# Performance work log

Measured on AMD Instinct MI355X. Metric: run time of the kernel, lower is better.

Reference implementation:

```python
import jax, jax.numpy as jnp
import numpy as np

N, T, F_IN = 20000, 6, 64   # nodes, seq_len, in_channels
E = 320000                  # edges (avg degree 16)
H, C = 4, 64                # gat1 heads, hidden_channels


def setup_inputs() -> dict:
    key = jax.random.key(0)
    ks = jax.random.split(key, 16)
    p = lambda i, shape, s=0.1: jax.random.normal(ks[i], shape, jnp.float32) * s
    return dict(
        x=p(0, (N, T, F_IN), 1.0),
        edge_index=jax.random.randint(ks[1], (2, E), 0, N),
        # GATv2 layer 1: in=F_IN, out=C per head, H heads, concat
        Wl1=p(2, (F_IN, H * C)), Wr1=p(3, (F_IN, H * C)), att1=p(4, (H, C)), b1=jnp.zeros((H * C,), jnp.float32),
        # GATv2 layer 2: in=H*C, out=C, 1 head, no concat
        Wl2=p(5, (H * C, C)), Wr2=p(6, (H * C, C)), att2=p(7, (1, C)), b2=jnp.zeros((C,), jnp.float32),
        # LSTM (input C, hidden C), pytorch gate order i,f,g,o
        Wih=p(8, (4 * C, C)), Whh=p(9, (4 * C, C)), bih=jnp.zeros((4 * C,), jnp.float32), bhh=jnp.zeros((4 * C,), jnp.float32),
        # MLP head
        Wfc1=p(10, (C, C // 2)), bfc1=jnp.zeros((C // 2,), jnp.float32),
        Wout=p(11, (C // 2, 1)), bout=jnp.zeros((1,), jnp.float32),
    )


def gatv2(xt, src, dst, Wl, Wr, att, bias, n):
    """GATv2Conv (eval mode, no edge_attr): gather -> attn -> segment-softmax -> scatter."""
    heads = att.shape[0]
    d = Wl.shape[1] // heads
    xl = (xt @ Wl).reshape(n, heads, d)   # source transform
    xr = (xt @ Wr).reshape(n, heads, d)   # target transform
    e = jax.nn.leaky_relu(xl[src] + xr[dst], 0.2)           # [E, heads, d]
    logit = jnp.einsum('ehc,hc->eh', e, att)                # [E, heads]
    m = jax.ops.segment_max(logit, dst, num_segments=n)      # per-target max
    ex = jnp.exp(logit - m[dst])
    denom = jax.ops.segment_sum(ex, dst, num_segments=n)
    alpha = ex / denom[dst]                                  # segment softmax
    out = jax.ops.segment_sum(alpha[:, :, None] * xl[src], dst, num_segments=n)
    return out.reshape(n, heads * d) + bias


def reference(x, edge_index, Wl1, Wr1, att1, b1, Wl2, Wr2, att2, b2,
              Wih, Whh, bih, bhh, Wfc1, bfc1, Wout, bout):
    src, dst = edge_index[0], edge_index[1]
    n = x.shape[0]

    def gat_step(carry, xt):                    # per-timestep spatial encoder
        h1 = jax.nn.elu(gatv2(xt, src, dst, Wl1, Wr1, att1, b1, n))
        h2 = jax.nn.elu(gatv2(h1, src, dst, Wl2, Wr2, att2, b2, n))
        return carry, h2

    _, seq = jax.lax.scan(gat_step, 0.0, jnp.swapaxes(x, 0, 1))  # [T, N, C]

    hid = Whh.shape[1]

    def lstm_step(carry, xt):
        h, c = carry
        g = xt @ Wih.T + bih + h @ Whh.T + bhh
        i, f, gg, o = jnp.split(g, 4, axis=-1)
        c = jax.nn.sigmoid(f) * c + jax.nn.sigmoid(i) * jnp.tanh(gg)
        h = jax.nn.sigmoid(o) * jnp.tanh(c)
        return (h, c), None

    h0 = jnp.zeros((n, hid), x.dtype)
    (h_last, _), _ = jax.lax.scan(lstm_step, (h0, h0), seq)

    z = jax.nn.relu(h_last @ Wfc1 + bfc1)
    return z @ Wout + bout
```

## Files before the change

### kernel.cpp

```cpp
#include <hip/hip_runtime.h>
#include <hip/hip_fp16.h>
#include <math.h>

#define N_NODES 20000
#define T_STEPS 6
#define F_INCH  64
#define HC      256
#define CH      64

typedef _Float16 h8    __attribute__((ext_vector_type(8)));
typedef _Float16 hv2   __attribute__((ext_vector_type(2)));
typedef float    f32x4 __attribute__((ext_vector_type(4)));

__device__ __forceinline__ float fast_tanh(float x){
  float e = __expf(2.f*x);
  return 1.f - 2.f/(e + 1.f);
}

__device__ __forceinline__ float fdot2v(hv2 a, hv2 b, float c){
#if __has_builtin(__builtin_amdgcn_fdot2)
  return __builtin_amdgcn_fdot2(a, b, c, false);
#else
  return fmaf((float)a[0], (float)b[0], fmaf((float)a[1], (float)b[1], c));
#endif
}

__device__ __forceinline__ hv2 leaky2(hv2 t){
  hv2 s = t * (_Float16)0.2f;
#if __has_builtin(__builtin_elementwise_max)
  return __builtin_elementwise_max(t, s);
#else
  hv2 r;
  r[0] = (t[0] > s[0]) ? t[0] : s[0];
  r[1] = (t[1] > s[1]) ? t[1] : s[1];
  return r;
#endif
}

__global__ void k_count(const int* __restrict__ dst, int E, int* __restrict__ deg){
  int e = blockIdx.x*256 + threadIdx.x;
  if (e < E) atomicAdd(&deg[dst[e]], 1);
}

__global__ void k_scan(const int* __restrict__ deg, int* __restrict__ row_start, int N){
  __shared__ int wsum[16];
  const int PT = 20;
  int tid = threadIdx.x, wid = tid >> 6, lane = tid & 63;
  int base = tid*PT;
  int loc[PT];
  int s = 0;
  #pragma unroll
  for (int j = 0; j < PT; j++){
    int i = base + j;
    int v = (i < N) ? deg[i] : 0;
    loc[j] = s;
    s += v;
  }
  int ss = s;
  #pragma unroll
  for (int off = 1; off < 64; off <<= 1){
    int t = __shfl_up(ss, off, 64);
    if (lane >= off) ss += t;
  }
  if (lane == 63) wsum[wid] = ss;
  __syncthreads();
  if (tid < 16){
    int w = wsum[tid];
    #pragma unroll
    for (int off = 1; off < 16; off <<= 1){
      int t = __shfl_up(w, off, 64);
      if (tid >= off) w += t;
    }
    wsum[tid] = w;
  }
  __syncthreads();
  int pre = ((wid ? wsum[wid-1] : 0)) + (ss - s);
  #pragma unroll
  for (int j = 0; j < PT; j++){
    int i = base + j;
    if (i < N) row_start[i] = pre + loc[j];
  }
  if (tid == 0) row_start[N] = wsum[15];
}

__global__ void k_scatter(const int* __restrict__ src, const int* __restrict__ dst, int E,
                          const int* __restrict__ row_start, int* __restrict__ cursor,
                          int* __restrict__ csr){
  int e = blockIdx.x*256 + threadIdx.x;
  if (e < E){
    int d = dst[e];
    int pos = atomicAdd(&cursor[d], 1);
    csr[row_start[d] + pos] = src[e];
  }
}

__global__ void k_sort(const int* __restrict__ row_start, int* __restrict__ csr, int N){
  int wid = threadIdx.x >> 6, lane = threadIdx.x & 63;
  int d = blockIdx.x*4 + wid;
  if (d >= N) return;
  int s = row_start[d], e = row_start[d+1], len = e - s;
  if (len <= 1) return;
  if (len <= 64){
    int v = (lane < len) ? csr[s + lane] : 0x7fffffff;
    int rank = 0;
    for (int j = 0; j < len; j++){
      int vj = __shfl(v, j, 64);
      rank += (int)((vj < v) | ((vj == v) & (j < lane)));
    }
    if (lane < len) csr[s + rank] = v;
  } else if (lane == 0){
    for (int i = s+1; i < e; i++){
      int key = csr[i]; int j = i-1;
      while (j >= s && csr[j] > key){ csr[j+1] = csr[j]; j--; }
      csr[j+1] = key;
    }
  }
}

__device__ __forceinline__ void packB_dev(const float* __restrict__ B, _Float16* __restrict__ Bf,
                                          int K, int N, int idx){
  if (idx >= K*N) return;
  int j    = idx & 7;
  int lane = (idx >> 3) & 63;
  int ntk  = idx >> 9;
  int NT = N >> 4;
  int ks = ntk / NT, nt = ntk - ks*NT;
  int k = ks*32 + ((lane >> 4) << 3) + j;
  int n = nt*16 + (lane & 15);
  Bf[idx] = (_Float16)B[k*N + n];
}

__device__ __forceinline__ void packBT_dev(const float* __restrict__ W, _Float16* __restrict__ Bf,
                                           int K, int N, int idx){
  if (idx >= K*N) return;
  int j    = idx & 7;
  int lane = (idx >> 3) & 63;
  int ntk  = idx >> 9;
  int NT = N >> 4;
  int ks = ntk / NT, nt = ntk - ks*NT;
  int k = ks*32 + ((lane >> 4) << 3) + j;
  int n = nt*16 + (lane & 15);
  Bf[idx] = (_Float16)W[n*K + k];
}

__global__ void k_packall(const float* __restrict__ bih, const float* __restrict__ bhh,
                          float* __restrict__ biasc,
                          const float* __restrict__ Wl1, _Float16* __restrict__ Bl1f,
                          const float* __restrict__ Wr1, _Float16* __restrict__ Br1f,
                          const float* __restrict__ Wl2, _Float16* __restrict__ Bl2f,
                          const float* __restrict__ Wr2, _Float16* __restrict__ Br2f,
                          const float* __restrict__ Wih, _Float16* __restrict__ Wihf,
                          const float* __restrict__ Whh, _Float16* __restrict__ Whhf){
  int grp = blockIdx.x >> 6;
  int idx = (blockIdx.x & 63)*256 + threadIdx.x;
  if (grp == 0){
    if (idx < 256) biasc[idx] = bih[idx] + bhh[idx];
  } else if (grp == 1){
    packB_dev(Wl1, Bl1f, 64, 256, idx);
  } else if (grp == 2){
    packB_dev(Wr1, Br1f, 64, 256, idx);
  } else if (grp == 3){
    packB_dev(Wl2, Bl2f, 256, 64, idx);
  } else if (grp == 4){
    packB_dev(Wr2, Br2f, 256, 64, idx);
  } else if (grp == 5){
    packBT_dev(Wih, Wihf, 64, 256, idx);
  } else {
    packBT_dev(Whh, Whhf, 64, 256, idx);
  }
}

__global__ __launch_bounds__(256) void k_gemm1_all(
    const float* __restrict__ x, const _Float16* __restrict__ B1f,
    const _Float16* __restrict__ B2f,
    __half* __restrict__ xl_all, __half* __restrict__ xr_all, int M){
  __shared__ _Float16 aT[32*72];
  int t = blockIdx.y;
  const float* A = x + t*F_INCH;
  _Float16* C1 = (_Float16*)(void*)xl_all + (size_t)t*N_NODES*HC;
  _Float16* C2 = (_Float16*)(void*)xr_all + (size_t)t*N_NODES*HC;
  int tid = threadIdx.x;
  int r0 = blockIdx.x*32;
  for (int i = tid; i < 32*64; i += 256){
    int r = i >> 6, k = i & 63;
    int row = r0 + r;
    aT[r*72 + k] = (row < M) ? (_Float16)A[(size_t)row*(T_STEPS*F_INCH) + k] : (_Float16)0.f;
  }
  __syncthreads();
  int wave = tid >> 6, lane = tid & 63;
  int m = wave & 1;
  const h8* Bfrag = (const h8*)((wave >> 1) ? B2f : B1f);
  _Float16* C = (wave >> 1) ? C2 : C1;
  int arow = m*16 + (lane & 15);
  int kb = (lane >> 4) * 8;
  h8 a0 = *(const h8*)&aT[arow*72 + kb];
  h8 a1 = *(const h8*)&aT[arow*72 + 32 + kb];
  f32x4 z = {0.f, 0.f, 0.f, 0.f};
  f32x4 acc[16];
  #pragma unroll
  for (int nt = 0; nt < 16; nt++) acc[nt] = z;
  #pragma unroll
  for (int nt = 0; nt < 16; nt++){
    h8 b0 = Bfrag[nt*64 + lane];
    h8 b1 = Bfrag[(16 + nt)*64 + lane];
    acc[nt] = __builtin_amdgcn_mfma_f32_16x16x32_f16(a0, b0, acc[nt], 0, 0, 0);
    acc[nt] = __builtin_amdgcn_mfma_f32_16x16x32_f16(a1, b1, acc[nt], 0, 0, 0);
  }
  int ccol = lane & 15, crow = (lane >> 4) * 4;
  #pragma unroll
  for (int nt = 0; nt < 16; nt++){
    #pragma unroll
    for (int r = 0; r < 4; r++){
      int row = r0 + m*16 + crow + r;
      if (row < M) C[(size_t)row*256 + nt*16 + ccol] = (_Float16)acc[nt][r];
    }
  }
}

__global__ __launch_bounds__(256) void k_gemm2_all(
    const __half* __restrict__ Aall, const _Float16* __restrict__ B1f,
    const _Float16* __restrict__ B2f,
    __half* __restrict__ C1h_all, __half* __restrict__ C2h_all, int M){
  __shared__ _Float16 aT[32*264];
  int t = blockIdx.y;
  const _Float16* A = (const _Float16*)(const void*)Aall + (size_t)t*N_NODES*HC;
  _Float16* C1 = (_Float16*)(void*)C1h_all + (size_t)t*N_NODES*CH;
  _Float16* C2 = (_Float16*)(void*)C2h_all + (size_t)t*N_NODES*CH;
  int tid = threadIdx.x;
  int r0 = blockIdx.x*32;
  h8 zh = {(_Float16)0.f,(_Float16)0.f,(_Float16)0.f,(_Float16)0.f,
           (_Float16)0.f,(_Float16)0.f,(_Float16)0.f,(_Float16)0.f};
  for (int i = tid; i < 32*32; i += 256){
    int r = i >> 5, c = i & 31;
    int row = r0 + r;
    h8 v = zh;
    if (row < M) v = *(const h8*)&A[(size_t)row*256 + c*8];
    *(h8*)&aT[r*264 + c*8] = v;
  }
  __syncthreads();
  int wave = tid >> 6, lane = tid & 63;
  int m = wave & 1;
  const h8* Bfrag = (const h8*)((wave >> 1) ? B2f : B1f);
  _Float16* C = (wave >> 1) ? C2 : C1;
  int arow = m*16 + (lane & 15);
  int kb = (lane >> 4) * 8;
  f32x4 z = {0.f, 0.f, 0.f, 0.f};
  f32x4 acc[4];
  #pragma unroll
  for (int nt = 0; nt < 4; nt++) acc[nt] = z;
  #pragma unroll
  for (int ks = 0; ks < 8; ks++){
    h8 a = *(const h8*)&aT[arow*264 + ks*32 + kb];
    #pragma unroll
    for (int nt = 0; nt < 4; nt++){
      h8 b = Bfrag[(ks*4 + nt)*64 + lane];
      acc[nt] = __builtin_amdgcn_mfma_f32_16x16x32_f16(a, b, acc[nt], 0, 0, 0);
    }
  }
  int ccol = lane & 15, crow = (lane >> 4) * 4;
  #pragma unroll
  for (int nt = 0; nt < 4; nt++){
    #pragma unroll
    for (int r = 0; r < 4; r++){
      int row = r0 + m*16 + crow + r;
      if (row < M) C[(size_t)row*64 + nt*16 + ccol] = (_Float16)acc[nt][r];
    }
  }
}

__global__ void k_gat1_all(const __half* __restrict__ xl_all, const __half* __restrict__ xr_all,
                           const int* __restrict__ row_start, const int* __restrict__ csr,
                           const float* __restrict__ att, const float* __restrict__ bias,
                           __half* __restrict__ out_all, int N){
  int wid = threadIdx.x >> 6, lane = threadIdx.x & 63;
  int dst = blockIdx.x*4 + wid;
  if (dst >= N) return;
  int t = blockIdx.y;
  const char* xlb = (const char*)(xl_all + (size_t)t*N_NODES*HC);
  const uint2* xrh = (const uint2*)(xr_all + (size_t)t*N_NODES*HC);
  uint2* outh = (uint2*)(out_all + (size_t)t*N_NODES*HC);
  uint2 xr_raw = xrh[(unsigned)(dst*64 + lane)];
  hv2 xr01 = *reinterpret_cast<hv2*>(&xr_raw.x);
  hv2 xr23 = *reinterpret_cast<hv2*>(&xr_raw.y);
  float4 at4 = ((const float4*)att)[lane];
  hv2 at01; at01[0] = (_Float16)at4.x; at01[1] = (_Float16)at4.y;
  hv2 at23; at23[0] = (_Float16)at4.z; at23[1] = (_Float16)at4.w;
  unsigned loff = lane*8u;
  int s0 = __builtin_amdgcn_readfirstlane(row_start[dst]);
  int s1 = __builtin_amdgcn_readfirstlane(row_start[dst+1]);
  float den = 0.f, ax = 0.f, ay = 0.f, az = 0.f, aw = 0.f;

  auto STEP = [&](uint2 raw){
    hv2 h01 = *reinterpret_cast<hv2*>(&raw.x);
    hv2 h23 = *reinterpret_cast<hv2*>(&raw.y);
    hv2 l01 = leaky2(h01 + xr01);
    hv2 l23 = leaky2(h23 + xr23);
    float p = fdot2v(l01, at01, fdot2v(l23, at23, 0.f));
    p += __shfl_xor(p, 1, 64);
    p += __shfl_xor(p, 2, 64);
    p += __shfl_xor(p, 4, 64);
    p += __shfl_xor(p, 8, 64);
    float w = __expf(p);
    den += w;
    ax = fmaf(w, (float)h01[0], ax);
    ay = fmaf(w, (float)h01[1], ay);
    az = fmaf(w, (float)h23[0], az);
    aw = fmaf(w, (float)h23[1], aw);
  };

  for (int base = s0; base < s1; base += 64){
    int rem = s1 - base;
    int cnt = rem < 64 ? rem : 64;
    int idxv = (base + lane < s1) ? csr[base + lane] : 0;
    auto LD = [&](int i)->uint2 {
      int s = __builtin_amdgcn_readlane(idxv, i & 63);
      return *(const uint2*)(xlb + (((size_t)(unsigned)s) << 9) + loff);
    };
    uint2 p0=LD(0), p1=LD(1), p2=LD(2), p3=LD(3);
    uint2 p4=LD(4), p5=LD(5), p6=LD(6), p7=LD(7);
    for (int i = 0; i < cnt; i += 4){
      uint2 n0=LD(i+8), n1=LD(i+9), n2=LD(i+10), n3=LD(i+11);
      if (i + 4 <= cnt){
        STEP(p0); STEP(p1); STEP(p2); STEP(p3);
      } else {
        STEP(p0);
        if (i+1 < cnt) STEP(p1);
        if (i+2 < cnt) STEP(p2);
        if (i+3 < cnt) STEP(p3);
      }
      p0=p4; p1=p5; p2=p6; p3=p7;
      p4=n0; p5=n1; p6=n2; p7=n3;
    }
  }
  float invd = (s1 > s0) ? 1.f/den : 0.f;
  float4 b4 = ((const float4*)bias)[lane];
  float rx = fmaf(ax, invd, b4.x);
  float ry = fmaf(ay, invd, b4.y);
  float rz = fmaf(az, invd, b4.z);
  float rw = fmaf(aw, invd, b4.w);
  rx = rx > 0.f ? rx : (__expf(rx) - 1.f);
  ry = ry > 0.f ? ry : (__expf(ry) - 1.f);
  rz = rz > 0.f ? rz : (__expf(rz) - 1.f);
  rw = rw > 0.f ? rw : (__expf(rw) - 1.f);
  __half2 o01 = __floats2half2_rn(rx, ry);
  __half2 o23 = __floats2half2_rn(rz, rw);
  uint2 o;
  o.x = *reinterpret_cast<unsigned int*>(&o01);
  o.y = *reinterpret_cast<unsigned int*>(&o23);
  outh[(unsigned)(dst*64 + lane)] = o;
}

__global__ void k_gat2_all(const __half* __restrict__ xl_all, const __half* __restrict__ xr_all,
                           const int* __restrict__ row_start, const int* __restrict__ csr,
                           const float* __restrict__ att, const float* __restrict__ bias,
                           __half* __restrict__ out_all, int N){
  int wid = threadIdx.x >> 6, lane = threadIdx.x & 63;
  int dst = blockIdx.x*4 + wid;
  if (dst >= N) return;
  int t = blockIdx.y;
  int g = lane >> 4, q = lane & 15;
  const char* xlb = (const char*)(xl_all + (size_t)t*N_NODES*CH);
  const uint2* xrh = (const uint2*)(xr_all + (size_t)t*N_NODES*CH);
  uint2* outh = (uint2*)(out_all + (size_t)t*N_NODES*CH);
  uint2 xr_raw = xrh[(unsigned)(dst*16 + q)];
  hv2 xr01 = *reinterpret_cast<hv2*>(&xr_raw.x);
  hv2 xr23 = *reinterpret_cast<hv2*>(&xr_raw.y);
  float4 at4 = ((const float4*)att)[q];
  hv2 at01; at01[0] = (_Float16)at4.x; at01[1] = (_Float16)at4.y;
  hv2 at23; at23[0] = (_Float16)at4.z; at23[1] = (_Float16)at4.w;
  unsigned qoff = q*8u;
  int s0 = __builtin_amdgcn_readfirstlane(row_start[dst]);
  int s1 = __builtin_amdgcn_readfirstlane(row_start[dst+1]);
  float den = 0.f, ax = 0.f, ay = 0.f, az = 0.f, aw = 0.f;

  for (int base = s0; base < s1; base += 64){
    int rem = s1 - base;
    int cnt = rem < 64 ? rem : 64;
    int idxv = (base + lane < s1) ? csr[base + lane] : 0;
    int K = (cnt + 3) >> 2;
    int e0 = g, e1 = g + 4;
    int sA = __shfl(idxv, e0 < cnt ? e0 : 0, 64);
    int sB = __shfl(idxv, e1 < cnt ? e1 : 0, 64);
    uint2 vA = *(const uint2*)(xlb + (((size_t)(unsigned)sA) << 7) + qoff);
    uint2 vB = *(const uint2*)(xlb + (((size_t)(unsigned)sB) << 7) + qoff);
    for (int k = 0; k < K; k++){
      int en = 4*k + 8 + g;
      int sN = __shfl(idxv, en < cnt ? en : 0, 64);
      uint2 vN = *(const uint2*)(xlb + (((size_t)(unsigned)sN) << 7) + qoff);
      int e = 4*k + g;
      if (e < cnt){
        hv2 h01 = *reinterpret_cast<hv2*>(&vA.x);
        hv2 h23 = *reinterpret_cast<hv2*>(&vA.y);
        hv2 l01 = leaky2(h01 + xr01);
        hv2 l23 = leaky2(h23 + xr23);
        float p = fdot2v(l01, at01, fdot2v(l23, at23, 0.f));
        p += __shfl_xor(p, 1, 64);
        p += __shfl_xor(p, 2, 64);
        p += __shfl_xor(p, 4, 64);
        p += __shfl_xor(p, 8, 64);
        float w = __expf(p);
        den += w;
        ax = fmaf(w, (float)h01[0], ax);
        ay = fmaf(w, (float)h01[1], ay);
        az = fmaf(w, (float)h23[0], az);
        aw = fmaf(w, (float)h23[1], aw);
      }
      vA = vB; vB = vN;
    }
  }
  den += __shfl_xor(den, 16, 64); den += __shfl_xor(den, 32, 64);
  ax  += __shfl_xor(ax, 16, 64);  ax  += __shfl_xor(ax, 32, 64);
  ay  += __shfl_xor(ay, 16, 64);  ay  += __shfl_xor(ay, 32, 64);
  az  += __shfl_xor(az, 16, 64);  az  += __shfl_xor(az, 32, 64);
  aw  += __shfl_xor(aw, 16, 64);  aw  += __shfl_xor(aw, 32, 64);
  float invd = (s1 > s0) ? 1.f/den : 0.f;
  float4 b4 = ((const float4*)bias)[q];
  float rx = fmaf(ax, invd, b4.x);
  float ry = fmaf(ay, invd, b4.y);
  float rz = fmaf(az, invd, b4.z);
  float rw = fmaf(aw, invd, b4.w);
  rx = rx > 0.f ? rx : (__expf(rx) - 1.f);
  ry = ry > 0.f ? ry : (__expf(ry) - 1.f);
  rz = rz > 0.f ? rz : (__expf(rz) - 1.f);
  rw = rw > 0.f ? rw : (__expf(rw) - 1.f);
  if (g == 0){
    __half2 o01 = __floats2half2_rn(rx, ry);
    __half2 o23 = __floats2half2_rn(rz, rw);
    uint2 o;
    o.x = *reinterpret_cast<unsigned int*>(&o01);
    o.y = *reinterpret_cast<unsigned int*>(&o23);
    outh[(unsigned)(dst*16 + q)] = o;
  }
}

__global__ __launch_bounds__(256) void k_gemmx_all(
    const __half* __restrict__ Aall, const _Float16* __restrict__ Bf,
    const float* __restrict__ biasc, __half* __restrict__ Call){
  __shared__ _Float16 aT[32*72];
  int tid = threadIdx.x;
  int r0 = blockIdx.x*32;
  {
    int r = tid >> 3, c8 = tid & 7;
    *(h8*)&aT[r*72 + c8*8] =
        *(const h8*)&((const _Float16*)(const void*)Aall)[((size_t)(r0+r))*64 + c8*8];
  }
  __syncthreads();
  int wave = tid >> 6, lane = tid & 63;
  int m = wave & 1, nh = wave >> 1;
  int arow = m*16 + (lane & 15);
  int kb = (lane >> 4) * 8;
  h8 a0 = *(const h8*)&aT[arow*72 + kb];
  h8 a1 = *(const h8*)&aT[arow*72 + 32 + kb];
  const h8* B = (const h8*)Bf;
  f32x4 z = {0.f, 0.f, 0.f, 0.f};
  f32x4 acc[8];
  #pragma unroll
  for (int nt = 0; nt < 8; nt++) acc[nt] = z;
  #pragma unroll
  for (int nt = 0; nt < 8; nt++){
    int ntg = nh*8 + nt;
    acc[nt] = __builtin_amdgcn_mfma_f32_16x16x32_f16(a0, B[ntg*64 + lane],        acc[nt], 0,0,0);
    acc[nt] = __builtin_amdgcn_mfma_f32_16x16x32_f16(a1, B[(16 + ntg)*64 + lane], acc[nt], 0,0,0);
  }
  int ccol = lane & 15, crow = (lane >> 4) * 4;
  _Float16* C = (_Float16*)(void*)Call;
  #pragma unroll
  for (int nt = 0; nt < 8; nt++){
    int ntg = nh*8 + nt;
    int col = ntg*16 + ccol;
    float b = biasc[col];
    #pragma unroll
    for (int r = 0; r < 4; r++){
      C[(size_t)(r0 + m*16 + crow + r)*256 + col] = (_Float16)(acc[nt][r] + b);
    }
  }
}

__global__ __launch_bounds__(64) void k_lstm_rec(
    const __half* __restrict__ gatesx,
    const _Float16* __restrict__ Whhf,
    const float* __restrict__ Wfc1, const float* __restrict__ bfc1,
    const float* __restrict__ Wout, const float* __restrict__ bout,
    float* __restrict__ out, int N){
  __shared__ _Float16 gxT[16*264];
  __shared__ _Float16 hT[16*68];
  int lane = threadIdx.x;
  int r0 = blockIdx.x*16;
  for (int i = lane; i < 16*68; i += 64) hT[i] = (_Float16)0.f;
  int ccol = lane & 15, crow = (lane >> 4) * 4;
  int arow_off = (lane & 15)*68 + ((lane >> 4) << 3);
  const h8* Bfrag = (const h8*)Whhf;
  const _Float16* gxb = (const _Float16*)(const void*)gatesx;
  float c[16];
  #pragma unroll
  for (int i = 0; i < 16; i++) c[i] = 0.f;

  for (int t = 0; t < T_STEPS; t++){
    const _Float16* gx = gxb + ((size_t)t*N_NODES + r0)*256;
    #pragma unroll
    for (int it = 0; it < 8; it++){
      int idx = it*64 + lane;
      int r = idx >> 5, c8 = idx & 31;
      *(h8*)&gxT[r*264 + c8*8] = *(const h8*)&gx[(size_t)r*256 + c8*8];
    }
    h8 a0 = *(const h8*)&hT[arow_off];
    h8 a1 = *(const h8*)&hT[arow_off + 32];
    f32x4 z = {0.f, 0.f, 0.f, 0.f};
    f32x4 acc[16];
    #pragma unroll
    for (int nt = 0; nt < 16; nt++) acc[nt] = z;
    #pragma unroll
    for (int nt = 0; nt < 16; nt++){
      acc[nt] = __builtin_amdgcn_mfma_f32_16x16x32_f16(a0, Bfrag[nt*64 + lane],        acc[nt], 0,0,0);
      acc[nt] = __builtin_amdgcn_mfma_f32_16x16x32_f16(a1, Bfrag[(16 + nt)*64 + lane], acc[nt], 0,0,0);
    }
    #pragma unroll
    for (int us = 0; us < 4; us++){
      int ucol = us*16 + ccol;
      #pragma unroll
      for (int r = 0; r < 4; r++){
        int row = crow + r;
        float gi = acc[us     ][r] + (float)gxT[row*264 +       ucol];
        float gf = acc[4  + us][r] + (float)gxT[row*264 +  64 + ucol];
        float gg = acc[8  + us][r] + (float)gxT[row*264 + 128 + ucol];
        float go = acc[12 + us][r] + (float)gxT[row*264 + 192 + ucol];
        float I = 1.f/(1.f + __expf(-gi));
        float F = 1.f/(1.f + __expf(-gf));
        float O = 1.f/(1.f + __expf(-go));
        float G = fast_tanh(gg);
        float cc = fmaf(F, c[us*4 + r], I*G);
        c[us*4 + r] = cc;
        hT[row*68 + ucol] = (_Float16)(O * fast_tanh(cc));
      }
    }
  }
  int rowm = lane >> 2;
  int cb = (lane & 3) * 8;
  float a8[8];
  #pragma unroll
  for (int j = 0; j < 8; j++) a8[j] = bfc1[cb + j];
  for (int k = 0; k < 64; k++){
    float hv = (float)hT[rowm*68 + k];
    #pragma unroll
    for (int j = 0; j < 8; j++) a8[j] = fmaf(hv, Wfc1[k*32 + cb + j], a8[j]);
  }
  float v = 0.f;
  #pragma unroll
  for (int j = 0; j < 8; j++) v += fmaxf(a8[j], 0.f) * Wout[cb + j];
  v += __shfl_xor(v, 1, 64);
  v += __shfl_xor(v, 2, 64);
  if ((lane & 3) == 0) out[r0 + rowm] = v + bout[0];
}

extern "C" void kernel_launch(void* const* d_in, const int* in_sizes, int n_in,
                              void* d_out, int out_size, void* d_ws, size_t ws_size,
                              hipStream_t stream){
  const float* x    = (const float*)d_in[0];
  const int*   edge = (const int*)  d_in[1];
  const float* Wl1  = (const float*)d_in[2];
  const float* Wr1  = (const float*)d_in[3];
  const float* att1 = (const float*)d_in[4];
  const float* b1   = (const float*)d_in[5];
  const float* Wl2  = (const float*)d_in[6];
  const float* Wr2  = (const float*)d_in[7];
  const float* att2 = (const float*)d_in[8];
  const float* b2   = (const float*)d_in[9];
  const float* Wih  = (const float*)d_in[10];
  const float* Whh  = (const float*)d_in[11];
  const float* bih  = (const float*)d_in[12];
  const float* bhh  = (const float*)d_in[13];
  const float* Wfc1 = (const float*)d_in[14];
  const float* bfc1 = (const float*)d_in[15];
  const float* Wout = (const float*)d_in[16];
  const float* bout = (const float*)d_in[17];
  float* out = (float*)d_out;

  const int N = N_NODES;
  const int E = in_sizes[1] / 2;

  char* p = (char*)d_ws;
  auto alloc = [&](size_t bytes)->char*{ char* q = p; p += (bytes + 255) & ~(size_t)255; return q; };
  int* csr       = (int*)alloc((size_t)E*sizeof(int));
  int* row_start = (int*)alloc((size_t)(N+1)*sizeof(int));
  int* deg       = (int*)alloc((size_t)N*sizeof(int));
  int* cursor    = (int*)alloc((size_t)N*sizeof(int));
  const size_t NB = (size_t)T_STEPS*N_NODES*HC;
  char* bufA = alloc(NB*2);
  char* bufB = alloc(NB*2);
  char* bufC = alloc(NB*2);
  float* biasc  = (float*)alloc(256*4);
  _Float16* Bl1f = (_Float16*)alloc(64*256*2);
  _Float16* Br1f = (_Float16*)alloc(64*256*2);
  _Float16* Bl2f = (_Float16*)alloc(256*64*2);
  _Float16* Br2f = (_Float16*)alloc(256*64*2);
  _Float16* Wihf = (_Float16*)alloc(64*256*2);
  _Float16* Whhf = (_Float16*)alloc(64*256*2);

  __half* xl1h_all = (__half*)bufA;
  __half* xr1h_all = (__half*)bufB;
  __half* h1_all   = (__half*)bufC;
  __half* xl2h_all = (__half*)bufA;
  __half* xr2h_all = (__half*)(bufA + (size_t)T_STEPS*N_NODES*CH*2);
  __half* h2f_all  = (__half*)bufB;
  __half* gatesx   = (__half*)bufC;

  const int* srcIdx = edge;
  const int* dstIdx = edge + E;

  hipMemsetAsync(deg, 0, (size_t)((char*)cursor - (char*)deg) + (size_t)N*4, stream);

  k_count  <<<(E+255)/256, 256, 0, stream>>>(dstIdx, E, deg);
  k_scan   <<<1, 1024, 0, stream>>>(deg, row_start, N);
  k_scatter<<<(E+255)/256, 256, 0, stream>>>(srcIdx, dstIdx, E, row_start, cursor, csr);
  k_sort   <<<(N+3)/4, 256, 0, stream>>>(row_start, csr, N);
  k_packall<<<448, 256, 0, stream>>>(bih, bhh, biasc,
                                     Wl1, Bl1f, Wr1, Br1f, Wl2, Bl2f, Wr2, Br2f,
                                     Wih, Wihf, Whh, Whhf);

  dim3 gGemm((N+31)/32, T_STEPS);
  dim3 gGat ((N+3)/4,  T_STEPS);
  k_gemm1_all<<<gGemm, 256, 0, stream>>>(x, Bl1f, Br1f, xl1h_all, xr1h_all, N);
  k_gat1_all <<<gGat,  256, 0, stream>>>(xl1h_all, xr1h_all, row_start, csr, att1, b1, h1_all, N);
  k_gemm2_all<<<gGemm, 256, 0, stream>>>(h1_all, Bl2f, Br2f, xl2h_all, xr2h_all, N);
  k_gat2_all <<<gGat,  256, 0, stream>>>(xl2h_all, xr2h_all, row_start, csr, att2, b2, h2f_all, N);

  k_gemmx_all<<<(T_STEPS*N)/32, 256, 0, stream>>>(h2f_all, Wihf, biasc, gatesx);
  k_lstm_rec <<<N/16, 64, 0, stream>>>(gatesx, Whhf, Wfc1, bfc1, Wout, bout, out, N);
}
```

Before: 403.3 us.

## Fuse LSTM input projection into recurrent kernel with concatenated Wih|Whh weights

Removes the separate gates-x GEMM kernel and its fp16 [T,N,256] intermediate. Each LSTM step now runs one K=128 MFMA over the concatenated [x_t, h] tile against a packed Wih|Whh matrix, with the bias held in registers. Each wave handles only 8 real rows padded to 16, so half the MFMA rows are wasted. Blocks become 256 threads with 4 independent waves. This trades the intermediate's memory traffic for extra compute inside the recurrence.

New measurement: 413.5 us. 1.03x slower.

```diff
diff --git a/kernel.cpp b/kernel.cpp
--- a/kernel.cpp
+++ b/kernel.cpp
@@ -130,17 +130,17 @@
   Bf[idx] = (_Float16)B[k*N + n];
 }
 
-__device__ __forceinline__ void packBT_dev(const float* __restrict__ W, _Float16* __restrict__ Bf,
-                                           int K, int N, int idx){
-  if (idx >= K*N) return;
+__device__ __forceinline__ void packWc_dev(const float* __restrict__ Wih,
+                                           const float* __restrict__ Whh,
+                                           _Float16* __restrict__ Wcf, int idx){
+  if (idx >= 128*256) return;
   int j    = idx & 7;
   int lane = (idx >> 3) & 63;
   int ntk  = idx >> 9;
-  int NT = N >> 4;
-  int ks = ntk / NT, nt = ntk - ks*NT;
+  int ks = ntk >> 4, nt = ntk & 15;
   int k = ks*32 + ((lane >> 4) << 3) + j;
   int n = nt*16 + (lane & 15);
-  Bf[idx] = (_Float16)W[n*K + k];
+  Wcf[idx] = (_Float16)((k < 64) ? Wih[n*64 + k] : Whh[n*64 + (k - 64)]);
 }
 
 __global__ void k_packall(const float* __restrict__ bih, const float* __restrict__ bhh,
@@ -149,8 +149,8 @@
                           const float* __restrict__ Wr1, _Float16* __restrict__ Br1f,
                           const float* __restrict__ Wl2, _Float16* __restrict__ Bl2f,
                           const float* __restrict__ Wr2, _Float16* __restrict__ Br2f,
-                          const float* __restrict__ Wih, _Float16* __restrict__ Wihf,
-                          const float* __restrict__ Whh, _Float16* __restrict__ Whhf){
+                          const float* __restrict__ Wih, const float* __restrict__ Whh,
+                          _Float16* __restrict__ Wcf){
   int grp = blockIdx.x >> 6;
   int idx = (blockIdx.x & 63)*256 + threadIdx.x;
   if (grp == 0){
@@ -164,9 +164,9 @@
   } else if (grp == 4){
     packB_dev(Wr2, Br2f, 256, 64, idx);
   } else if (grp == 5){
-    packBT_dev(Wih, Wihf, 64, 256, idx);
+    packWc_dev(Wih, Whh, Wcf, idx);
   } else {
-    packBT_dev(Whh, Whhf, 64, 256, idx);
+    packWc_dev(Wih, Whh, Wcf, idx + 16384);
   }
 }
 
@@ -433,123 +433,97 @@
   }
 }
 
-__global__ __launch_bounds__(256) void k_gemmx_all(
-    const __half* __restrict__ Aall, const _Float16* __restrict__ Bf,
-    const float* __restrict__ biasc, __half* __restrict__ Call){
-  __shared__ _Float16 aT[32*72];
-  int tid = threadIdx.x;
-  int r0 = blockIdx.x*32;
-  {
-    int r = tid >> 3, c8 = tid & 7;
-    *(h8*)&aT[r*72 + c8*8] =
-        *(const h8*)&((const _Float16*)(const void*)Aall)[((size_t)(r0+r))*64 + c8*8];
-  }
-  __syncthreads();
-  int wave = tid >> 6, lane = tid & 63;
-  int m = wave & 1, nh = wave >> 1;
-  int arow = m*16 + (lane & 15);
-  int kb = (lane >> 4) * 8;
-  h8 a0 = *(const h8*)&aT[arow*72 + kb];
-  h8 a1 = *(const h8*)&aT[arow*72 + 32 + kb];
-  const h8* B = (const h8*)Bf;
-  f32x4 z = {0.f, 0.f, 0.f, 0.f};
-  f32x4 acc[8];
-  #pragma unroll
-  for (int nt = 0; nt < 8; nt++) acc[nt] = z;
-  #pragma unroll
-  for (int nt = 0; nt < 8; nt++){
-    int ntg = nh*8 + nt;
-    acc[nt] = __builtin_amdgcn_mfma_f32_16x16x32_f16(a0, B[ntg*64 + lane],        acc[nt], 0,0,0);
-    acc[nt] = __builtin_amdgcn_mfma_f32_16x16x32_f16(a1, B[(16 + ntg)*64 + lane], acc[nt], 0,0,0);
-  }
-  int ccol = lane & 15, crow = (lane >> 4) * 4;
-  _Float16* C = (_Float16*)(void*)Call;
-  #pragma unroll
-  for (int nt = 0; nt < 8; nt++){
-    int ntg = nh*8 + nt;
-    int col = ntg*16 + ccol;
-    float b = biasc[col];
-    #pragma unroll
-    for (int r = 0; r < 4; r++){
-      C[(size_t)(r0 + m*16 + crow + r)*256 + col] = (_Float16)(acc[nt][r] + b);
-    }
-  }
-}
-
-__global__ __launch_bounds__(64) void k_lstm_rec(
-    const __half* __restrict__ gatesx,
-    const _Float16* __restrict__ Whhf,
+__global__ __launch_bounds__(256) void k_lstm_rec(
+    const __half* __restrict__ h2f_all,
+    const _Float16* __restrict__ Wcf,
+    const float* __restrict__ biasc,
     const float* __restrict__ Wfc1, const float* __restrict__ bfc1,
     const float* __restrict__ Wout, const float* __restrict__ bout,
     float* __restrict__ out, int N){
-  __shared__ _Float16 gxT[16*264];
-  __shared__ _Float16 hT[16*68];
-  int lane = threadIdx.x;
-  int r0 = blockIdx.x*16;
-  for (int i = lane; i < 16*68; i += 64) hT[i] = (_Float16)0.f;
+  __shared__ _Float16 aT[4][16*136];
+  int tid = threadIdx.x;
+  int w = tid >> 6, lane = tid & 63;
+  int r0 = blockIdx.x*32 + w*8;
+  _Float16* A = aT[w];
+  for (int i = lane; i < 16*136; i += 64) A[i] = (_Float16)0.f;
   int ccol = lane & 15, crow = (lane >> 4) * 4;
-  int arow_off = (lane & 15)*68 + ((lane >> 4) << 3);
-  const h8* Bfrag = (const h8*)Whhf;
-  const _Float16* gxb = (const _Float16*)(const void*)gatesx;
+  bool valid = crow < 8;
+  int arow = lane & 15;
+  int kb = (lane >> 4) * 8;
+  float bi4[4], bf4[4], bg4[4], bo4[4];
+  #pragma unroll
+  for (int us = 0; us < 4; us++){
+    int u = us*16 + ccol;
+    bi4[us] = biasc[u];
+    bf4[us] = biasc[64 + u];
+    bg4[us] = biasc[128 + u];
+    bo4[us] = biasc[192 + u];
+  }
+  const h8* B = (const h8*)Wcf;
+  const _Float16* h2b = (const _Float16*)(const void*)h2f_all;
   float c[16];
   #pragma unroll
   for (int i = 0; i < 16; i++) c[i] = 0.f;
 
   for (int t = 0; t < T_STEPS; t++){
-    const _Float16* gx = gxb + ((size_t)t*N_NODES + r0)*256;
-    #pragma unroll
-    for (int it = 0; it < 8; it++){
-      int idx = it*64 + lane;
-      int r = idx >> 5, c8 = idx & 31;
-      *(h8*)&gxT[r*264 + c8*8] = *(const h8*)&gx[(size_t)r*256 + c8*8];
-    }
-    h8 a0 = *(const h8*)&hT[arow_off];
-    h8 a1 = *(const h8*)&hT[arow_off + 32];
+    {
+      int r = lane >> 3, c8 = lane & 7;
+      *(h8*)&A[r*136 + c8*8] = *(const h8*)&h2b[((size_t)t*N_NODES + r0 + r)*64 + c8*8];
+    }
+    h8 a0 = *(const h8*)&A[arow*136 +  0 + kb];
+    h8 a1 = *(const h8*)&A[arow*136 + 32 + kb];
+    h8 a2 = *(const h8*)&A[arow*136 + 64 + kb];
+    h8 a3 = *(const h8*)&A[arow*136 + 96 + kb];
     f32x4 z = {0.f, 0.f, 0.f, 0.f};
     f32x4 acc[16];
     #pragma unroll
     for (int nt = 0; nt < 16; nt++) acc[nt] = z;
     #pragma unroll
     for (int nt = 0; nt < 16; nt++){
-      acc[nt] = __builtin_amdgcn_mfma_f32_16x16x32_f16(a0, Bfrag[nt*64 + lane],        acc[nt], 0,0,0);
-      acc[nt] = __builtin_amdgcn_mfma_f32_16x16x32_f16(a1, Bfrag[(16 + nt)*64 + lane], acc[nt], 0,0,0);
-    }
+      acc[nt] = __builtin_amdgcn_mfma_f32_16x16x32_f16(a0, B[nt*64 + lane],        acc[nt], 0,0,0);
+      acc[nt] = __builtin_amdgcn_mfma_f32_16x16x32_f16(a1, B[(16+nt)*64 + lane],   acc[nt], 0,0,0);
+      acc[nt] = __builtin_amdgcn_mfma_f32_16x16x32_f16(a2, B[(32+nt)*64 + lane],   acc[nt], 0,0,0);
+      acc[nt] = __builtin_amdgcn_mfma_f32_16x16x32_f16(a3, B[(48+nt)*64 + lane],   acc[nt], 0,0,0);
+    }
+    if (valid){
+      #pragma unroll
+      for (int us = 0; us < 4; us++){
+        int ucol = us*16 + ccol;
+        #pragma unroll
+        for (int r = 0; r < 4; r++){
+          int row = crow + r;
+          float gi = acc[us     ][r] + bi4[us];
+          float gf = acc[4  + us][r] + bf4[us];
+          float gg = acc[8  + us][r] + bg4[us];
+          float go = acc[12 + us][r] + bo4[us];
+          float I = 1.f/(1.f + __expf(-gi));
+          float F = 1.f/(1.f + __expf(-gf));
+          float O = 1.f/(1.f + __expf(-go));
+          float G = fast_tanh(gg);
+          float cc = fmaf(F, c[us*4 + r], I*G);
+          c[us*4 + r] = cc;
+          A[row*136 + 64 + ucol] = (_Float16)(O * fast_tanh(cc));
+        }
+      }
+    }
+  }
+  int rowm = lane >> 3;
+  int cb = (lane & 7) * 4;
+  float a4[4];
+  #pragma unroll
+  for (int j = 0; j < 4; j++) a4[j] = bfc1[cb + j];
+  for (int k = 0; k < 64; k++){
+    float hv = (float)A[rowm*136 + 64 + k];
     #pragma unroll
-    for (int us = 0; us < 4; us++){
-      int ucol = us*16 + ccol;
-      #pragma unroll
-      for (int r = 0; r < 4; r++){
-        int row = crow + r;
-        float gi = acc[us     ][r] + (float)gxT[row*264 +       ucol];
-        float gf = acc[4  + us][r] + (float)gxT[row*264 +  64 + ucol];
-        float gg = acc[8  + us][r] + (float)gxT[row*264 + 128 + ucol];
-        float go = acc[12 + us][r] + (float)gxT[row*264 + 192 + ucol];
-        float I = 1.f/(1.f + __expf(-gi));
-        float F = 1.f/(1.f + __expf(-gf));
-        float O = 1.f/(1.f + __expf(-go));
-        float G = fast_tanh(gg);
-        float cc = fmaf(F, c[us*4 + r], I*G);
-        c[us*4 + r] = cc;
-        hT[row*68 + ucol] = (_Float16)(O * fast_tanh(cc));
-      }
-    }
-  }
-  int rowm = lane >> 2;
-  int cb = (lane & 3) * 8;
-  float a8[8];
-  #pragma unroll
-  for (int j = 0; j < 8; j++) a8[j] = bfc1[cb + j];
-  for (int k = 0; k < 64; k++){
-    float hv = (float)hT[rowm*68 + k];
-    #pragma unroll
-    for (int j = 0; j < 8; j++) a8[j] = fmaf(hv, Wfc1[k*32 + cb + j], a8[j]);
+    for (int j = 0; j < 4; j++) a4[j] = fmaf(hv, Wfc1[k*32 + cb + j], a4[j]);
   }
   float v = 0.f;
   #pragma unroll
-  for (int j = 0; j < 8; j++) v += fmaxf(a8[j], 0.f) * Wout[cb + j];
+  for (int j = 0; j < 4; j++) v += fmaxf(a4[j], 0.f) * Wout[cb + j];
   v += __shfl_xor(v, 1, 64);
   v += __shfl_xor(v, 2, 64);
-  if ((lane & 3) == 0) out[r0 + rowm] = v + bout[0];
+  v += __shfl_xor(v, 4, 64);
+  if ((lane & 7) == 0) out[r0 + rowm] = v + bout[0];
 }
 
 extern "C" void kernel_launch(void* const* d_in, const int* in_sizes, int n_in,
@@ -593,8 +567,7 @@
   _Float16* Br1f = (_Float16*)alloc(64*256*2);
   _Float16* Bl2f = (_Float16*)alloc(256*64*2);
   _Float16* Br2f = (_Float16*)alloc(256*64*2);
-  _Float16* Wihf = (_Float16*)alloc(64*256*2);
-  _Float16* Whhf = (_Float16*)alloc(64*256*2);
+  _Float16* Wcf  = (_Float16*)alloc(128*256*2);
 
   __half* xl1h_all = (__half*)bufA;
   __half* xr1h_all = (__half*)bufB;
@@ -602,7 +575,6 @@
   __half* xl2h_all = (__half*)bufA;
   __half* xr2h_all = (__half*)(bufA + (size_t)T_STEPS*N_NODES*CH*2);
   __half* h2f_all  = (__half*)bufB;
-  __half* gatesx   = (__half*)bufC;
 
   const int* srcIdx = edge;
   const int* dstIdx = edge + E;
@@ -615,7 +587,7 @@
   k_sort   <<<(N+3)/4, 256, 0, stream>>>(row_start, csr, N);
   k_packall<<<448, 256, 0, stream>>>(bih, bhh, biasc,
                                      Wl1, Bl1f, Wr1, Br1f, Wl2, Bl2f, Wr2, Br2f,
-                                     Wih, Wihf, Whh, Whhf);
+                                     Wih, Whh, Wcf);
 
   dim3 gGemm((N+31)/32, T_STEPS);
   dim3 gGat ((N+3)/4,  T_STEPS);
@@ -624,6 +596,5 @@
   k_gemm2_all<<<gGemm, 256, 0, stream>>>(h1_all, Bl2f, Br2f, xl2h_all, xr2h_all, N);
   k_gat2_all <<<gGat,  256, 0, stream>>>(xl2h_all, xr2h_all, row_start, csr, att2, b2, h2f_all, N);
 
-  k_gemmx_all<<<(T_STEPS*N)/32, 256, 0, stream>>>(h2f_all, Wihf, biasc, gatesx);
-  k_lstm_rec <<<N/16, 64, 0, stream>>>(gatesx, Whhf, Wfc1, bfc1, Wout, bout, out, N);
-}
+  k_lstm_rec<<<N/32, 256, 0, stream>>>(h2f_all, Wcf, biasc, Wfc1, bfc1, Wout, bout, out, N);
+}
```

## Stage LSTM recurrent weights in LDS shared by four waves, 8 rows per wave

Applied to the files above, without the earlier changes.

The LSTM recurrence kernel now runs 256-thread blocks in which the Whh MFMA fragments are loaded once into padded shared memory and reused by four waves, instead of each 64-thread block reading them from global/L2 every timestep. Each wave handles 8 node rows while still issuing 16-row MFMAs; the upper half of the tile is zero padding and its outputs are discarded. This cuts weight traffic but doubles the MFMA work per node and raises LDS use per block, which may reduce occupancy.

Result: slower. 465.1 us (+15.3%).

```diff
diff --git a/kernel.cpp b/kernel.cpp
--- a/kernel.cpp
+++ b/kernel.cpp
@@ -476,80 +476,94 @@
   }
 }
 
-__global__ __launch_bounds__(64) void k_lstm_rec(
+__global__ __launch_bounds__(256) void k_lstm_rec(
     const __half* __restrict__ gatesx,
     const _Float16* __restrict__ Whhf,
     const float* __restrict__ Wfc1, const float* __restrict__ bfc1,
     const float* __restrict__ Wout, const float* __restrict__ bout,
     float* __restrict__ out, int N){
-  __shared__ _Float16 gxT[16*264];
-  __shared__ _Float16 hT[16*68];
-  int lane = threadIdx.x;
-  int r0 = blockIdx.x*16;
-  for (int i = lane; i < 16*68; i += 64) hT[i] = (_Float16)0.f;
+  __shared__ _Float16 BS[2048*8 + 2048];
+  __shared__ _Float16 aT[4][16*72];
+  __shared__ _Float16 gxT[4][8*264];
+  int tid = threadIdx.x, w = tid >> 6, lane = tid & 63;
+  int r0 = blockIdx.x*32 + w*8;
+  for (int i = tid; i < 2048; i += 256){
+    *(h8*)&BS[i*8 + ((i >> 3) << 3)] = *(const h8*)&Whhf[(size_t)i*8];
+  }
+  _Float16* A  = aT[w];
+  _Float16* GX = gxT[w];
+  for (int i = lane; i < 16*72; i += 64) A[i] = (_Float16)0.f;
+  __syncthreads();
   int ccol = lane & 15, crow = (lane >> 4) * 4;
-  int arow_off = (lane & 15)*68 + ((lane >> 4) << 3);
-  const h8* Bfrag = (const h8*)Whhf;
+  bool valid = crow < 8;
+  int arow = lane & 15;
+  int kb = (lane >> 4) * 8;
   const _Float16* gxb = (const _Float16*)(const void*)gatesx;
   float c[16];
   #pragma unroll
   for (int i = 0; i < 16; i++) c[i] = 0.f;
 
   for (int t = 0; t < T_STEPS; t++){
-    const _Float16* gx = gxb + ((size_t)t*N_NODES + r0)*256;
-    #pragma unroll
-    for (int it = 0; it < 8; it++){
+    #pragma unroll
+    for (int it = 0; it < 4; it++){
       int idx = it*64 + lane;
       int r = idx >> 5, c8 = idx & 31;
-      *(h8*)&gxT[r*264 + c8*8] = *(const h8*)&gx[(size_t)r*256 + c8*8];
-    }
-    h8 a0 = *(const h8*)&hT[arow_off];
-    h8 a1 = *(const h8*)&hT[arow_off + 32];
+      *(h8*)&GX[r*264 + c8*8] = *(const h8*)&gxb[((size_t)t*N_NODES + r0 + r)*256 + c8*8];
+    }
+    h8 a0 = *(const h8*)&A[arow*72 + kb];
+    h8 a1 = *(const h8*)&A[arow*72 + 32 + kb];
     f32x4 z = {0.f, 0.f, 0.f, 0.f};
     f32x4 acc[16];
     #pragma unroll
     for (int nt = 0; nt < 16; nt++) acc[nt] = z;
     #pragma unroll
     for (int nt = 0; nt < 16; nt++){
-      acc[nt] = __builtin_amdgcn_mfma_f32_16x16x32_f16(a0, Bfrag[nt*64 + lane],        acc[nt], 0,0,0);
-      acc[nt] = __builtin_amdgcn_mfma_f32_16x16x32_f16(a1, Bfrag[(16 + nt)*64 + lane], acc[nt], 0,0,0);
-    }
-    #pragma unroll
-    for (int us = 0; us < 4; us++){
-      int ucol = us*16 + ccol;
+      int i0 = nt*64 + lane;
+      int i1 = (16 + nt)*64 + lane;
+      h8 b0 = *(const h8*)&BS[i0*8 + ((i0 >> 3) << 3)];
+      h8 b1 = *(const h8*)&BS[i1*8 + ((i1 >> 3) << 3)];
+      acc[nt] = __builtin_amdgcn_mfma_f32_16x16x32_f16(a0, b0, acc[nt], 0, 0, 0);
+      acc[nt] = __builtin_amdgcn_mfma_f32_16x16x32_f16(a1, b1, acc[nt], 0, 0, 0);
+    }
+    if (valid){
       #pragma unroll
-      for (int r = 0; r < 4; r++){
-        int row = crow + r;
-        float gi = acc[us     ][r] + (float)gxT[row*264 +       ucol];
-        float gf = acc[4  + us][r] + (float)gxT[row*264 +  64 + ucol];
-        float gg = acc[8  + us][r] + (float)gxT[row*264 + 128 + ucol];
-        float go = acc[12 + us][r] + (float)gxT[row*264 + 192 + ucol];
-        float I = 1.f/(1.f + __expf(-gi));
-        float F = 1.f/(1.f + __expf(-gf));
-        float O = 1.f/(1.f + __expf(-go));
-        float G = fast_tanh(gg);
-        float cc = fmaf(F, c[us*4 + r], I*G);
-        c[us*4 + r] = cc;
-        hT[row*68 + ucol] = (_Float16)(O * fast_tanh(cc));
+      for (int us = 0; us < 4; us++){
+        int ucol = us*16 + ccol;
+        #pragma unroll
+        for (int r = 0; r < 4; r++){
+          int row = crow + r;
+          float gi = acc[us     ][r] + (float)GX[row*264 +       ucol];
+          float gf = acc[4  + us][r] + (float)GX[row*264 +  64 + ucol];
+          float gg = acc[8  + us][r] + (float)GX[row*264 + 128 + ucol];
+          float go = acc[12 + us][r] + (float)GX[row*264 + 192 + ucol];
+          float I = 1.f/(1.f + __expf(-gi));
+          float F = 1.f/(1.f + __expf(-gf));
+          float O = 1.f/(1.f + __expf(-go));
+          float G = fast_tanh(gg);
+          float cc = fmaf(F, c[us*4 + r], I*G);
+          c[us*4 + r] = cc;
+          A[row*72 + ucol] = (_Float16)(O * fast_tanh(cc));
+        }
       }
     }
   }
-  int rowm = lane >> 2;
-  int cb = (lane & 3) * 8;
-  float a8[8];
-  #pragma unroll
-  for (int j = 0; j < 8; j++) a8[j] = bfc1[cb + j];
+  int rowm = lane >> 3;
+  int cb = (lane & 7) * 4;
+  float a4[4];
+  #pragma unroll
+  for (int j = 0; j < 4; j++) a4[j] = bfc1[cb + j];
   for (int k = 0; k < 64; k++){
-    float hv = (float)hT[rowm*68 + k];
-    #pragma unroll
-    for (int j = 0; j < 8; j++) a8[j] = fmaf(hv, Wfc1[k*32 + cb + j], a8[j]);
+    float hv = (float)A[rowm*72 + k];
+    #pragma unroll
+    for (int j = 0; j < 4; j++) a4[j] = fmaf(hv, Wfc1[k*32 + cb + j], a4[j]);
   }
   float v = 0.f;
   #pragma unroll
-  for (int j = 0; j < 8; j++) v += fmaxf(a8[j], 0.f) * Wout[cb + j];
+  for (int j = 0; j < 4; j++) v += fmaxf(a4[j], 0.f) * Wout[cb + j];
   v += __shfl_xor(v, 1, 64);
   v += __shfl_xor(v, 2, 64);
-  if ((lane & 3) == 0) out[r0 + rowm] = v + bout[0];
+  v += __shfl_xor(v, 4, 64);
+  if ((lane & 7) == 0) out[r0 + rowm] = v + bout[0];
 }
 
 extern "C" void kernel_launch(void* const* d_in, const int* in_sizes, int n_in,
@@ -625,5 +639,5 @@
   k_gat2_all <<<gGat,  256, 0, stream>>>(xl2h_all, xr2h_all, row_start, csr, att2, b2, h2f_all, N);
 
   k_gemmx_all<<<(T_STEPS*N)/32, 256, 0, stream>>>(h2f_all, Wihf, biasc, gatesx);
-  k_lstm_rec <<<N/16, 64, 0, stream>>>(gatesx, Whhf, Wfc1, bfc1, Wout, bout, out, N);
-}
+  k_lstm_rec <<<N/32, 256, 0, stream>>>(gatesx, Whhf, Wfc1, bfc1, Wout, bout, out, N);
+}
```
